# Optimization experiments

Hardware: AMD Instinct MI355X
Metric: run time of the kernel (lower is better)

The kernel has to match this reference:

```python
import jax, jax.numpy as jnp
import numpy as np

B, T, D, H, V, NPOS, NDEP, OUT = 65536, 7, 100, 700, 32000, 50, 45, 93


def setup_inputs() -> dict:
    key = jax.random.key(0)
    ks = jax.random.split(key, 16)
    word_idx = jax.random.randint(ks[0], (B, T), 0, V, dtype=jnp.int64)
    drop = jax.random.uniform(ks[1], (B, T)) < 0.05
    word_idx = jnp.where(drop, -1, word_idx)
    pos_idx = jax.random.randint(ks[2], (B, T), 0, NPOS, dtype=jnp.int32)
    dep_idx = jax.random.randint(ks[3], (B, T), 0, NDEP, dtype=jnp.int32)
    s = 0.05
    return {
        "word_idx": word_idx,
        "pos_idx": pos_idx,
        "dep_idx": dep_idx,
        "word_table": jax.random.normal(ks[4], (V, D), jnp.float32) * s,
        "pos_table": jax.random.normal(ks[5], (NPOS, D), jnp.float32) * s,
        "dep_table": jax.random.normal(ks[6], (NDEP, D), jnp.float32) * s,
        "Ww": jax.random.normal(ks[7], (T * D, H), jnp.float32) * s,
        "bw": jax.random.normal(ks[8], (H,), jnp.float32) * s,
        "Wp": jax.random.normal(ks[9], (T * D, H), jnp.float32) * s,
        "bp": jax.random.normal(ks[10], (H,), jnp.float32) * s,
        "Wd": jax.random.normal(ks[11], (T * D, H), jnp.float32) * s,
        "bd": jax.random.normal(ks[12], (H,), jnp.float32) * s,
        "Wo": jax.random.normal(ks[13], (H, OUT), jnp.float32) * s,
        "bo": jax.random.normal(ks[14], (OUT,), jnp.float32) * s,
    }


def reference(word_idx, pos_idx, dep_idx, word_table, pos_table, dep_table,
              Ww, bw, Wp, bp, Wd, bd, Wo, bo):
    b = word_idx.shape[0]
    # word lookup with -1 -> zeros (the '_' token), batched gather instead of
    # per-token loop + serial torch.cat
    we = jnp.where((word_idx >= 0)[..., None],
                   word_table[jnp.clip(word_idx, 0)], 0.0)          # [B,T,D]
    we = we.reshape(b, -1)                                           # [B,700]
    pe = pos_table[pos_idx].reshape(b, -1)                           # [B,700]
    de = dep_table[dep_idx].reshape(b, -1)                           # [B,700]
    h = (we @ Ww + bw) + (pe @ Wp + bp) + (de @ Wd + bd)             # [B,700]
    h = h * h * h                                                    # torch.pow(., 3)
    logits = h @ Wo + bo                                             # [B,OUT]
    # original applies Softmax(dim=0) to a 1-D [OUT] vector per example;
    # batched equivalent is softmax over the class axis
    return jax.nn.softmax(logits, axis=-1)
```

## Files before the change

### kernel.cpp

```cpp
#include <hip/hip_runtime.h>
#include <stdint.h>

#define BM 64
#define NTT 44
#define KSTEPS 43
#define KE 1376
#define H3S 360
#define OUTC 93
#define KS2 22

typedef __attribute__((ext_vector_type(8))) short bf16x8;
typedef __attribute__((ext_vector_type(4))) float f32x4;

#define O_WB   0
#define SZ_WB  (KSTEPS*NTT*64*8*2)
#define O_WOP  (O_WB + SZ_WB)
#define SZ_WOP (KS2*6*64*8*2)

__device__ __forceinline__ unsigned short f2bf(float f) {
  unsigned u = __float_as_uint(f);
  u += 0x7FFFu + ((u >> 16) & 1u);
  return (unsigned short)(u >> 16);
}

__global__ void pack_w(const float* __restrict__ W, unsigned short* __restrict__ out,
                       int Ksrc, int Nsrc, int ntiles) {
  int blk = blockIdx.x;
  int ks = blk / ntiles, nt = blk - ks*ntiles;
  int l = threadIdx.x;
  int n = nt*16 + (l & 15);
  int k0 = ks*32 + ((l >> 4) << 3);
  unsigned short v[8];
#pragma unroll
  for (int j = 0; j < 8; ++j) {
    int k = k0 + j;
    float f = (k < Ksrc && n < Nsrc) ? W[k*Nsrc + n] : 0.f;
    v[j] = f2bf(f);
  }
  ((uint4*)out)[blk*64 + l] = *(const uint4*)v;
}

__global__ void build_WB(const float* __restrict__ Ww, const float* __restrict__ Wp,
                         const float* __restrict__ Wd, const float* __restrict__ pos_table,
                         const float* __restrict__ dep_table, const float* __restrict__ bw,
                         const float* __restrict__ bp, const float* __restrict__ bd,
                         unsigned short* __restrict__ out) {
  int blk = blockIdx.x;
  int ks = blk / 11, q = blk - ks*11;
  int l = threadIdx.x & 63;
  int nt = q*4 + (threadIdx.x >> 6);
  int n = nt*16 + (l & 15);
  int k0 = ks*32 + ((l >> 4) << 3);
  unsigned short v[8];
#pragma unroll
  for (int j = 0; j < 8; ++j) {
    int k = k0 + j;
    float val = 0.f;
    if (n < 700) {
      if (k < 700) {
        val = Ww[k*700 + n];
      } else if (k < 1050) {
        int u = k - 700; int t = u/50; int p = u - t*50;
        const float* tr = pos_table + p*100;
        const float* wc = Wp + (t*100)*700 + n;
        float a = 0.f;
#pragma unroll 4
        for (int d = 0; d < 100; ++d) a += tr[d] * wc[d*700];
        val = a;
      } else if (k < 1365) {
        int u = k - 1050; int t = u/45; int dd = u - t*45;
        const float* tr = dep_table + dd*100;
        const float* wc = Wd + (t*100)*700 + n;
        float a = 0.f;
#pragma unroll 4
        for (int d = 0; d < 100; ++d) a += tr[d] * wc[d*700];
        val = a;
      } else if (k == 1365) {
        val = bw[n] + bp[n] + bd[n];
      }
    }
    v[j] = f2bf(val);
  }
  ((uint4*)out)[(ks*NTT + nt)*64 + l] = *(const uint4*)v;
}

struct SMem {
  union {
    struct { unsigned short A[4*64*8]; unsigned short B[NTT*64*8]; } mm;
    unsigned short h3h[64*H3S];
  } u;
  unsigned short widx[64][8];
  unsigned char  pidx[64][8];
  unsigned char  didx[64][8];
  float bo_l[96];
};

__launch_bounds__(512, 4)
__global__ void dp_main(const int* __restrict__ word_idx,
                        const int* __restrict__ pos_idx,
                        const int* __restrict__ dep_idx,
                        const float* __restrict__ word_table,
                        const unsigned short* __restrict__ WB,
                        const unsigned short* __restrict__ WoP,
                        const float* __restrict__ bo,
                        float* __restrict__ out) {
  __shared__ SMem sm;
  const int tid = threadIdx.x;
  const int lane = tid & 63;
  const int w = tid >> 6;
  const int blockRow = blockIdx.x * BM;

  if (tid < 448) {
    int r = tid / 7, t = tid - r*7;
    int g = (blockRow + r)*7 + t;
    int wi = word_idx[g];
    sm.widx[r][t] = (wi < 0) ? 0xFFFFu : (unsigned short)wi;
    sm.pidx[r][t] = (unsigned char)pos_idx[g];
    sm.didx[r][t] = (unsigned char)dep_idx[g];
  }
  if (tid < 96) sm.bo_l[tid] = (tid < OUTC) ? bo[tid] : 0.f;

  const int amt   = tid >> 7;
  const int alane = (tid >> 1) & 63;
  const int ahalf = tid & 1;
  const int arow  = amt*16 + (alane & 15);
  const int ak    = ((alane >> 4) << 3) + ahalf*4;

  const int mtb = (w >> 2) * 2;
  const int ntb = (w & 3) * 11;

  f32x4 acc0[11], acc1[11];
#pragma unroll
  for (int j = 0; j < 11; ++j) { acc0[j] = (f32x4){0,0,0,0}; acc1[j] = (f32x4){0,0,0,0}; }

  auto issueB = [&](int ks) {
    const unsigned short* src = WB + (size_t)ks*(NTT*64*8);
#pragma unroll
    for (int it = 0; it < 6; ++it) {
      int slot = it*512 + tid;
      if (slot < NTT*64) {
        __builtin_amdgcn_global_load_lds(
            (const __attribute__((address_space(1))) unsigned int*)(src + slot*8),
            (__attribute__((address_space(3))) unsigned int*)(sm.u.mm.B + slot*8),
            16, 0, 0);
      }
    }
  };
  auto stage1 = [&](int ks, float4& g) {
    int k0 = ks*32 + ak;
    g = make_float4(0.f, 0.f, 0.f, 0.f);
    if (k0 < 700) {
      int t = k0/100, d = k0 - t*100;
      unsigned wi = sm.widx[arow][t];
      if (wi != 0xFFFFu) g = *(const float4*)(word_table + (size_t)wi*100 + d);
    } else {
      unsigned short r_[4];
#pragma unroll
      for (int j = 0; j < 4; ++j) {
        int k = k0 + j;
        unsigned short rv = 0;
        if (k < 1050) {
          int u = k - 700; int t = u/50; int pp = u - t*50;
          if (pp == (int)sm.pidx[arow][t]) rv = 0x3F80;
        } else if (k < 1365) {
          int u = k - 1050; int t = u/45; int dd = u - t*45;
          if (dd == (int)sm.didx[arow][t]) rv = 0x3F80;
        } else if (k == 1365) rv = 0x3F80;
        r_[j] = rv;
      }
      g.x = __uint_as_float((unsigned)r_[0] | ((unsigned)r_[1] << 16));
      g.y = __uint_as_float((unsigned)r_[2] | ((unsigned)r_[3] << 16));
    }
  };
  auto stage2 = [&](int ks, float4 g) {
    int k0 = ks*32 + ak;
    unsigned v0, v1;
    if (k0 < 700) {
      v0 = (unsigned)f2bf(g.x) | ((unsigned)f2bf(g.y) << 16);
      v1 = (unsigned)f2bf(g.z) | ((unsigned)f2bf(g.w) << 16);
    } else {
      v0 = __float_as_uint(g.x);
      v1 = __float_as_uint(g.y);
    }
    uint2 pk; pk.x = v0; pk.y = v1;
    *(uint2*)(sm.u.mm.A + ((amt*64 + alane)*8 + ahalf*4)) = pk;
  };
  auto compute = [&]() {
    const bf16x8* Af = (const bf16x8*)sm.u.mm.A;
    const bf16x8* Bf = (const bf16x8*)sm.u.mm.B;
    bf16x8 a0 = Af[(mtb + 0)*64 + lane];
    bf16x8 a1 = Af[(mtb + 1)*64 + lane];
#pragma unroll
    for (int j = 0; j < 11; ++j) {
      bf16x8 b = Bf[(ntb + j)*64 + lane];
      acc0[j] = __builtin_amdgcn_mfma_f32_16x16x32_bf16(a0, b, acc0[j], 0, 0, 0);
      acc1[j] = __builtin_amdgcn_mfma_f32_16x16x32_bf16(a1, b, acc1[j], 0, 0, 0);
    }
  };

  issueB(0);
  __syncthreads();
  {
    float4 g; stage1(0, g); stage2(0, g);
  }
  __syncthreads();

  for (int ks = 0; ks < KSTEPS; ++ks) {
    float4 gn;
    const bool pre = (ks + 1 < KSTEPS);
    if (pre) stage1(ks + 1, gn);
    compute();
    __syncthreads();
    if (pre) { issueB(ks + 1); stage2(ks + 1, gn); }
    __syncthreads();
  }

  f32x4 c2[3];
#pragma unroll
  for (int jn = 0; jn < 3; ++jn) c2[jn] = (f32x4){0,0,0,0};
  const int mt2 = w >> 1;
  const int nb2 = (w & 1)*3;
  const int arow2 = mt2*16 + (lane & 15);
  const int koff2 = (lane >> 4)*8;
  const bf16x8* WoF = (const bf16x8*)WoP;
  const int myph = (w & 3) >> 1;
  const int lr = ((lane >> 4) << 2), lc = lane & 15;

#pragma unroll
  for (int ph = 0; ph < 2; ++ph) {
    if (myph == ph) {
      int cbase = ntb*16 - ph*352;
#pragma unroll
      for (int j = 0; j < 11; ++j) {
#pragma unroll
        for (int r = 0; r < 4; ++r) {
          float h0 = acc0[j][r];
          float h1 = acc1[j][r];
          sm.u.h3h[((mtb+0)*16 + lr + r)*H3S + cbase + j*16 + lc] = f2bf(h0*h0*h0);
          sm.u.h3h[((mtb+1)*16 + lr + r)*H3S + cbase + j*16 + lc] = f2bf(h1*h1*h1);
        }
      }
    }
    __syncthreads();
#pragma unroll 2
    for (int ksl = 0; ksl < 11; ++ksl) {
      bf16x8 a = *(const bf16x8*)(sm.u.h3h + arow2*H3S + ksl*32 + koff2);
      int ks2 = ph*11 + ksl;
#pragma unroll
      for (int jn = 0; jn < 3; ++jn) {
        bf16x8 b = WoF[(size_t)(ks2*6 + nb2 + jn)*64 + lane];
        c2[jn] = __builtin_amdgcn_mfma_f32_16x16x32_bf16(a, b, c2[jn], 0, 0, 0);
      }
    }
    __syncthreads();
  }

  {
    float* lg = (float*)sm.u.h3h;
#pragma unroll
    for (int jn = 0; jn < 3; ++jn)
#pragma unroll
      for (int r = 0; r < 4; ++r)
        lg[(mt2*16 + lr + r)*96 + (nb2 + jn)*16 + lc] = c2[jn][r];
  }
  __syncthreads();
  {
    const float* lg = (const float*)sm.u.h3h;
    int row = tid >> 3, s = tid & 7;
    const float4* lp = (const float4*)(lg + row*96 + s*12);
    float4 xa = lp[0], xb = lp[1], xc = lp[2];
    float x[12] = {xa.x,xa.y,xa.z,xa.w, xb.x,xb.y,xb.z,xb.w, xc.x,xc.y,xc.z,xc.w};
    int cb = s*12;
    float mx = -1e30f;
#pragma unroll
    for (int i = 0; i < 12; ++i) {
      int c = cb + i;
      x[i] += sm.bo_l[c];
      mx = fmaxf(mx, (c < OUTC) ? x[i] : -1e30f);
    }
    mx = fmaxf(mx, __shfl_xor(mx, 1, 8));
    mx = fmaxf(mx, __shfl_xor(mx, 2, 8));
    mx = fmaxf(mx, __shfl_xor(mx, 4, 8));
    float e[12]; float sum = 0.f;
#pragma unroll
    for (int i = 0; i < 12; ++i) {
      int c = cb + i;
      e[i] = (c < OUTC) ? __expf(x[i] - mx) : 0.f;
      sum += e[i];
    }
    sum += __shfl_xor(sum, 1, 8);
    sum += __shfl_xor(sum, 2, 8);
    sum += __shfl_xor(sum, 4, 8);
    float inv = 1.0f / sum;
    float* op = out + (size_t)(blockRow + row)*OUTC;
#pragma unroll
    for (int i = 0; i < 12; ++i) {
      int c = cb + i;
      if (c < OUTC) op[c] = e[i]*inv;
    }
  }
}

extern "C" void kernel_launch(void* const* d_in, const int* in_sizes, int n_in,
                              void* d_out, int out_size, void* d_ws, size_t ws_size,
                              hipStream_t stream) {
  const int*   word_idx   = (const int*)d_in[0];
  const int*   pos_idx    = (const int*)d_in[1];
  const int*   dep_idx    = (const int*)d_in[2];
  const float* word_table = (const float*)d_in[3];
  const float* pos_table  = (const float*)d_in[4];
  const float* dep_table  = (const float*)d_in[5];
  const float* Ww = (const float*)d_in[6];
  const float* bw = (const float*)d_in[7];
  const float* Wp = (const float*)d_in[8];
  const float* bp = (const float*)d_in[9];
  const float* Wd = (const float*)d_in[10];
  const float* bd = (const float*)d_in[11];
  const float* Wo = (const float*)d_in[12];
  const float* bo = (const float*)d_in[13];
  float* out = (float*)d_out;

  char* ws = (char*)d_ws;
  unsigned short* WBp = (unsigned short*)(ws + O_WB);
  unsigned short* WoP = (unsigned short*)(ws + O_WOP);

  build_WB<<<KSTEPS*11, 256, 0, stream>>>(Ww, Wp, Wd, pos_table, dep_table, bw, bp, bd, WBp);
  pack_w<<<KS2*6, 64, 0, stream>>>(Wo, WoP, 700, OUTC, 6);
  dp_main<<<65536/BM, 512, 0, stream>>>(word_idx, pos_idx, dep_idx, word_table,
                                        WBp, WoP, bo, out);
}
```

Baseline: 333.2 us.

## Double main kernel to 1024 threads and parallelize weight folding per element

The main kernel now runs 16 waves per block instead of 8. Each wave owns one 16-row M tile rather than two, which halves the accumulator registers per thread. The output GEMM is split unevenly across the extra waves. The folded-weight build kernel now uses one thread per bf16 element instead of eight, so more threads work on the pos/dep table folding. Word-table loads and softmax stores use nontemporal hints. The trade-off: each B tile in LDS is reused by only one A tile per wave, and the launch bound of 8 waves per SIMD may force register spilling or limit occupancy to one block per CU.

```diff
diff --git a/kernel.cpp b/kernel.cpp
--- a/kernel.cpp
+++ b/kernel.cpp
@@ -4,13 +4,13 @@
 #define BM 64
 #define NTT 44
 #define KSTEPS 43
-#define KE 1376
 #define H3S 360
 #define OUTC 93
 #define KS2 22
 
 typedef __attribute__((ext_vector_type(8))) short bf16x8;
 typedef __attribute__((ext_vector_type(4))) float f32x4;
+typedef __attribute__((ext_vector_type(4))) float fvec4;
 
 #define O_WB   0
 #define SZ_WB  (KSTEPS*NTT*64*8*2)
@@ -45,43 +45,40 @@
                          const float* __restrict__ dep_table, const float* __restrict__ bw,
                          const float* __restrict__ bp, const float* __restrict__ bd,
                          unsigned short* __restrict__ out) {
-  int blk = blockIdx.x;
-  int ks = blk / 11, q = blk - ks*11;
-  int l = threadIdx.x & 63;
-  int nt = q*4 + (threadIdx.x >> 6);
+  int id = blockIdx.x*256 + threadIdx.x;
+  if (id >= KSTEPS*NTT*64*8) return;
+  int j   = id & 7;
+  int l   = (id >> 3) & 63;
+  int rem = id >> 9;
+  int nt  = rem % NTT;
+  int ks  = rem / NTT;
+  int k = ks*32 + ((l >> 4) << 3) + j;
   int n = nt*16 + (l & 15);
-  int k0 = ks*32 + ((l >> 4) << 3);
-  unsigned short v[8];
-#pragma unroll
-  for (int j = 0; j < 8; ++j) {
-    int k = k0 + j;
-    float val = 0.f;
-    if (n < 700) {
-      if (k < 700) {
-        val = Ww[k*700 + n];
-      } else if (k < 1050) {
-        int u = k - 700; int t = u/50; int p = u - t*50;
-        const float* tr = pos_table + p*100;
-        const float* wc = Wp + (t*100)*700 + n;
-        float a = 0.f;
+  float val = 0.f;
+  if (n < 700) {
+    if (k < 700) {
+      val = Ww[k*700 + n];
+    } else if (k < 1050) {
+      int u = k - 700; int t = u/50; int p = u - t*50;
+      const float* tr = pos_table + p*100;
+      const float* wc = Wp + (t*100)*700 + n;
+      float a = 0.f;
 #pragma unroll 4
-        for (int d = 0; d < 100; ++d) a += tr[d] * wc[d*700];
-        val = a;
-      } else if (k < 1365) {
-        int u = k - 1050; int t = u/45; int dd = u - t*45;
-        const float* tr = dep_table + dd*100;
-        const float* wc = Wd + (t*100)*700 + n;
-        float a = 0.f;
+      for (int d = 0; d < 100; ++d) a += tr[d] * wc[d*700];
+      val = a;
+    } else if (k < 1365) {
+      int u = k - 1050; int t = u/45; int dd = u - t*45;
+      const float* tr = dep_table + dd*100;
+      const float* wc = Wd + (t*100)*700 + n;
+      float a = 0.f;
 #pragma unroll 4
-        for (int d = 0; d < 100; ++d) a += tr[d] * wc[d*700];
-        val = a;
-      } else if (k == 1365) {
-        val = bw[n] + bp[n] + bd[n];
-      }
-    }
-    v[j] = f2bf(val);
-  }
-  ((uint4*)out)[(ks*NTT + nt)*64 + l] = *(const uint4*)v;
+      for (int d = 0; d < 100; ++d) a += tr[d] * wc[d*700];
+      val = a;
+    } else if (k == 1365) {
+      val = bw[n] + bp[n] + bd[n];
+    }
+  }
+  out[id] = f2bf(val);
 }
 
 struct SMem {
@@ -95,7 +92,7 @@
   float bo_l[96];
 };
 
-__launch_bounds__(512, 4)
+__launch_bounds__(1024, 8)
 __global__ void dp_main(const int* __restrict__ word_idx,
                         const int* __restrict__ pos_idx,
                         const int* __restrict__ dep_idx,
@@ -126,18 +123,19 @@
   const int arow  = amt*16 + (alane & 15);
   const int ak    = ((alane >> 4) << 3) + ahalf*4;
 
-  const int mtb = (w >> 2) * 2;
-  const int ntb = (w & 3) * 11;
-
-  f32x4 acc0[11], acc1[11];
-#pragma unroll
-  for (int j = 0; j < 11; ++j) { acc0[j] = (f32x4){0,0,0,0}; acc1[j] = (f32x4){0,0,0,0}; }
+  const int mt  = w >> 2;
+  const int ng  = w & 3;
+  const int ntb = ng * 11;
+
+  f32x4 acc[11];
+#pragma unroll
+  for (int j = 0; j < 11; ++j) acc[j] = (f32x4){0,0,0,0};
 
   auto issueB = [&](int ks) {
     const unsigned short* src = WB + (size_t)ks*(NTT*64*8);
 #pragma unroll
-    for (int it = 0; it < 6; ++it) {
-      int slot = it*512 + tid;
+    for (int it = 0; it < 3; ++it) {
+      int slot = it*1024 + tid;
       if (slot < NTT*64) {
         __builtin_amdgcn_global_load_lds(
             (const __attribute__((address_space(1))) unsigned int*)(src + slot*8),
@@ -146,13 +144,14 @@
       }
     }
   };
-  auto stage1 = [&](int ks, float4& g) {
+  auto stage1 = [&](int ks, fvec4& g) {
     int k0 = ks*32 + ak;
-    g = make_float4(0.f, 0.f, 0.f, 0.f);
+    g = (fvec4){0.f, 0.f, 0.f, 0.f};
     if (k0 < 700) {
       int t = k0/100, d = k0 - t*100;
       unsigned wi = sm.widx[arow][t];
-      if (wi != 0xFFFFu) g = *(const float4*)(word_table + (size_t)wi*100 + d);
+      if (wi != 0xFFFFu)
+        g = __builtin_nontemporal_load((const fvec4*)(word_table + (size_t)wi*100 + d));
     } else {
       unsigned short r_[4];
 #pragma unroll
@@ -168,19 +167,19 @@
         } else if (k == 1365) rv = 0x3F80;
         r_[j] = rv;
       }
-      g.x = __uint_as_float((unsigned)r_[0] | ((unsigned)r_[1] << 16));
-      g.y = __uint_as_float((unsigned)r_[2] | ((unsigned)r_[3] << 16));
+      g[0] = __uint_as_float((unsigned)r_[0] | ((unsigned)r_[1] << 16));
+      g[1] = __uint_as_float((unsigned)r_[2] | ((unsigned)r_[3] << 16));
     }
   };
-  auto stage2 = [&](int ks, float4 g) {
+  auto stage2 = [&](int ks, fvec4 g) {
     int k0 = ks*32 + ak;
     unsigned v0, v1;
     if (k0 < 700) {
-      v0 = (unsigned)f2bf(g.x) | ((unsigned)f2bf(g.y) << 16);
-      v1 = (unsigned)f2bf(g.z) | ((unsigned)f2bf(g.w) << 16);
+      v0 = (unsigned)f2bf(g[0]) | ((unsigned)f2bf(g[1]) << 16);
+      v1 = (unsigned)f2bf(g[2]) | ((unsigned)f2bf(g[3]) << 16);
     } else {
-      v0 = __float_as_uint(g.x);
-      v1 = __float_as_uint(g.y);
+      v0 = __float_as_uint(g[0]);
+      v1 = __float_as_uint(g[1]);
     }
     uint2 pk; pk.x = v0; pk.y = v1;
     *(uint2*)(sm.u.mm.A + ((amt*64 + alane)*8 + ahalf*4)) = pk;
@@ -188,56 +187,51 @@
   auto compute = [&]() {
     const bf16x8* Af = (const bf16x8*)sm.u.mm.A;
     const bf16x8* Bf = (const bf16x8*)sm.u.mm.B;
-    bf16x8 a0 = Af[(mtb + 0)*64 + lane];
-    bf16x8 a1 = Af[(mtb + 1)*64 + lane];
+    bf16x8 a = Af[mt*64 + lane];
 #pragma unroll
     for (int j = 0; j < 11; ++j) {
       bf16x8 b = Bf[(ntb + j)*64 + lane];
-      acc0[j] = __builtin_amdgcn_mfma_f32_16x16x32_bf16(a0, b, acc0[j], 0, 0, 0);
-      acc1[j] = __builtin_amdgcn_mfma_f32_16x16x32_bf16(a1, b, acc1[j], 0, 0, 0);
+      acc[j] = __builtin_amdgcn_mfma_f32_16x16x32_bf16(a, b, acc[j], 0, 0, 0);
     }
   };
 
   issueB(0);
   __syncthreads();
-  {
-    float4 g; stage1(0, g); stage2(0, g);
-  }
+  if (tid < 512) { fvec4 g; stage1(0, g); stage2(0, g); }
   __syncthreads();
 
   for (int ks = 0; ks < KSTEPS; ++ks) {
-    float4 gn;
+    fvec4 gn;
     const bool pre = (ks + 1 < KSTEPS);
-    if (pre) stage1(ks + 1, gn);
+    if (pre && tid < 512) stage1(ks + 1, gn);
     compute();
     __syncthreads();
-    if (pre) { issueB(ks + 1); stage2(ks + 1, gn); }
+    if (pre) { issueB(ks + 1); if (tid < 512) stage2(ks + 1, gn); }
     __syncthreads();
   }
 
-  f32x4 c2[3];
-#pragma unroll
-  for (int jn = 0; jn < 3; ++jn) c2[jn] = (f32x4){0,0,0,0};
-  const int mt2 = w >> 1;
-  const int nb2 = (w & 1)*3;
+  f32x4 c2[2];
+  c2[0] = (f32x4){0,0,0,0}; c2[1] = (f32x4){0,0,0,0};
+  const int mt2 = w >> 2;
+  const int g2  = w & 3;
+  const int nstart = (g2 < 2) ? (g2*2) : (g2 + 2);
+  const int ncnt   = (g2 < 2) ? 2 : 1;
   const int arow2 = mt2*16 + (lane & 15);
   const int koff2 = (lane >> 4)*8;
   const bf16x8* WoF = (const bf16x8*)WoP;
-  const int myph = (w & 3) >> 1;
+  const int myph = ng >> 1;
   const int lr = ((lane >> 4) << 2), lc = lane & 15;
 
 #pragma unroll
   for (int ph = 0; ph < 2; ++ph) {
     if (myph == ph) {
-      int cbase = ntb*16 - ph*352;
+      int cbase = ng*176 - ph*352;
 #pragma unroll
       for (int j = 0; j < 11; ++j) {
 #pragma unroll
         for (int r = 0; r < 4; ++r) {
-          float h0 = acc0[j][r];
-          float h1 = acc1[j][r];
-          sm.u.h3h[((mtb+0)*16 + lr + r)*H3S + cbase + j*16 + lc] = f2bf(h0*h0*h0);
-          sm.u.h3h[((mtb+1)*16 + lr + r)*H3S + cbase + j*16 + lc] = f2bf(h1*h1*h1);
+          float h = acc[j][r];
+          sm.u.h3h[(mt*16 + lr + r)*H3S + cbase + j*16 + lc] = f2bf(h*h*h);
         }
       }
     }
@@ -247,9 +241,11 @@
       bf16x8 a = *(const bf16x8*)(sm.u.h3h + arow2*H3S + ksl*32 + koff2);
       int ks2 = ph*11 + ksl;
 #pragma unroll
-      for (int jn = 0; jn < 3; ++jn) {
-        bf16x8 b = WoF[(size_t)(ks2*6 + nb2 + jn)*64 + lane];
-        c2[jn] = __builtin_amdgcn_mfma_f32_16x16x32_bf16(a, b, c2[jn], 0, 0, 0);
+      for (int jn = 0; jn < 2; ++jn) {
+        if (jn < ncnt) {
+          bf16x8 b = WoF[(size_t)(ks2*6 + nstart + jn)*64 + lane];
+          c2[jn] = __builtin_amdgcn_mfma_f32_16x16x32_bf16(a, b, c2[jn], 0, 0, 0);
+        }
       }
     }
     __syncthreads();
@@ -258,13 +254,16 @@
   {
     float* lg = (float*)sm.u.h3h;
 #pragma unroll
-    for (int jn = 0; jn < 3; ++jn)
-#pragma unroll
-      for (int r = 0; r < 4; ++r)
-        lg[(mt2*16 + lr + r)*96 + (nb2 + jn)*16 + lc] = c2[jn][r];
+    for (int jn = 0; jn < 2; ++jn) {
+      if (jn < ncnt) {
+#pragma unroll
+        for (int r = 0; r < 4; ++r)
+          lg[(mt2*16 + lr + r)*96 + (nstart + jn)*16 + lc] = c2[jn][r];
+      }
+    }
   }
   __syncthreads();
-  {
+  if (tid < 512) {
     const float* lg = (const float*)sm.u.h3h;
     int row = tid >> 3, s = tid & 7;
     const float4* lp = (const float4*)(lg + row*96 + s*12);
@@ -296,7 +295,7 @@
 #pragma unroll
     for (int i = 0; i < 12; ++i) {
       int c = cb + i;
-      if (c < OUTC) op[c] = e[i]*inv;
+      if (c < OUTC) __builtin_nontemporal_store(e[i]*inv, op + c);
     }
   }
 }
@@ -324,8 +323,9 @@
   unsigned short* WBp = (unsigned short*)(ws + O_WB);
   unsigned short* WoP = (unsigned short*)(ws + O_WOP);
 
-  build_WB<<<KSTEPS*11, 256, 0, stream>>>(Ww, Wp, Wd, pos_table, dep_table, bw, bp, bd, WBp);
+  build_WB<<<(KSTEPS*NTT*64*8 + 255)/256, 256, 0, stream>>>(
+      Ww, Wp, Wd, pos_table, dep_table, bw, bp, bd, WBp);
   pack_w<<<KS2*6, 64, 0, stream>>>(Wo, WoP, 700, OUTC, 6);
-  dp_main<<<65536/BM, 512, 0, stream>>>(word_idx, pos_idx, dep_idx, word_table,
-                                        WBp, WoP, bo, out);
-}
+  dp_main<<<65536/BM, 1024, 0, stream>>>(word_idx, pos_idx, dep_idx, word_table,
+                                         WBp, WoP, bo, out);
+}
```

Result: slower. 653.2 us (+96.1%).
